# Performance work log

Measured on AMD Instinct MI355X. Metric: run time of the kernel, lower is better.

The kernel has to match this reference:

```python
import jax, jax.numpy as jnp
import numpy as np

THRESHOLD = 1.0  # LIF firing threshold (single-step LIF: spike = heaviside(v - thr))


def _lif_spike(v):
    # single-step LIF: membrane = input, spike where membrane exceeds threshold
    return (v > THRESHOLD).astype(v.dtype)


def setup_inputs() -> dict:
    key = jax.random.key(0)
    ks = jax.random.split(key, 9)
    B, T, C = 2, 2048, 1024
    s = 1.0 / np.sqrt(C)
    return {
        "x": jax.random.normal(ks[0], (B, T, C), dtype=jnp.float32),
        "Wq": jax.random.normal(ks[1], (C, C), dtype=jnp.float32) * s,
        "bq": jnp.zeros((C,), dtype=jnp.float32),
        "Wk": jax.random.normal(ks[2], (C, C), dtype=jnp.float32) * s,
        "bk": jnp.zeros((C,), dtype=jnp.float32),
        "Wv": jax.random.normal(ks[3], (C, C), dtype=jnp.float32) * s,
        "bv": jnp.zeros((C,), dtype=jnp.float32),
        "Wo": jax.random.normal(ks[4], (C, C), dtype=jnp.float32) * s,
        "bo": jnp.zeros((C,), dtype=jnp.float32),
    }


def reference(x, Wq, bq, Wk, bk, Wv, bv, Wo, bo):
    B, T, C = x.shape
    H = 16
    D = C // H
    q = x @ Wq.T + bq
    k = x @ Wk.T + bk
    v = x @ Wv.T + bv
    # LIF spiking on q and k (binary spikes)
    qs = _lif_spike(q).reshape(B, T, H, D).transpose(0, 2, 1, 3)  # [B,H,T,D]
    ks = _lif_spike(k).reshape(B, T, H, D).transpose(0, 2, 1, 3)  # [B,H,T,D]
    vh = v.reshape(B, T, H, D).transpose(0, 2, 1, 3)              # [B,H,T,D]
    scores = jnp.einsum('bhqd,bhkd->bhqk', qs, ks) / jnp.sqrt(jnp.asarray(D, x.dtype))
    attn = jax.nn.softmax(scores, axis=-1)
    out = jnp.einsum('bhqk,bhkd->bhqd', attn, vh)                 # [B,H,T,D]
    out = out.transpose(0, 2, 1, 3).reshape(B, T, C)
    return out @ Wo.T + bo
```

## Files before the change

### kernel.cpp

```cpp
#include <hip/hip_runtime.h>
#include <cstdint>

typedef unsigned long long u64;
typedef unsigned int u32;
typedef unsigned short u16;
typedef __attribute__((ext_vector_type(8))) u16 u16x8;
typedef __attribute__((ext_vector_type(4))) u16 u16x4;
typedef __attribute__((ext_vector_type(2))) u64 u64x2;
typedef __attribute__((ext_vector_type(8))) _Float16 f16x8;
typedef __attribute__((ext_vector_type(4))) float f32x4;

#define T_LEN 2048
#define C_DIM 1024
#define H_NUM 16
#define M_ROWS 4096
#define MB (1024ull * 1024ull)
#define TAU 3e-3f
#define FCAP 65536u
#define BLK_FCAP 512u

__device__ __forceinline__ u16 f2bf(float f) {
  unsigned u = __builtin_bit_cast(unsigned, f);
  return (u16)((u + 0x7FFFu + ((u >> 16) & 1u)) >> 16);
}
__device__ __forceinline__ u16 f2h(float f) {
  _Float16 h = (_Float16)f;
  return __builtin_bit_cast(u16, h);
}

__device__ __forceinline__ void async16(u16* lds, const u16* g) {
  __builtin_amdgcn_global_load_lds(
      (const __attribute__((address_space(1))) void*)g,
      (__attribute__((address_space(3))) void*)lds, 16, 0, 0);
}

__global__ __launch_bounds__(256) void split_all(
    const float* __restrict__ x,  const float* __restrict__ Wq,
    const float* __restrict__ Wk, const float* __restrict__ Wv,
    const float* __restrict__ Wo,
    u16* xh, u16* wq16, u16* wk16, u16* wv16, u16* woh, u32* flagcnt)
{
  const int i = blockIdx.x * 256 + threadIdx.x;
  if (i == 0) *flagcnt = 0;
  const float* src; u16* dst; int off; int isbf = 0;
  if      (i < 1048576) { src = x;  dst = xh;   off = i; }
  else if (i < 1310720) { src = Wq; dst = wq16; off = i - 1048576; }
  else if (i < 1572864) { src = Wk; dst = wk16; off = i - 1310720; }
  else if (i < 1835008) { src = Wv; dst = wv16; off = i - 1572864; }
  else                  { src = Wo; dst = woh;  off = i - 1835008; isbf = 1; }
  const float4 v = ((const float4*)src)[off];
  u16x4 h;
  if (isbf) {
    h[0] = f2bf(v.x); h[1] = f2bf(v.y); h[2] = f2bf(v.z); h[3] = f2bf(v.w);
  } else {
    h[0] = f2h(v.x);  h[1] = f2h(v.y);  h[2] = f2h(v.z);  h[3] = f2h(v.w);
  }
  ((u16x4*)dst)[off] = h;
}

__global__ __launch_bounds__(256) void mfma_qkv(
    const u16* __restrict__ A16,
    const u16* __restrict__ Bq16, const u16* __restrict__ Bk16,
    const u16* __restrict__ Bv16,
    const float* __restrict__ bq, const float* __restrict__ bk,
    const float* __restrict__ bv,
    u32* __restrict__ pbits, u32* __restrict__ flagcnt,
    u32* __restrict__ flaglist, u16* __restrict__ vT)
{
  __shared__ u16 Ahs[2][128][32];
  __shared__ u16 Bhs[2][128][32];
  __shared__ u32 fls[2 + BLK_FCAP];

  const int tid  = threadIdx.x;
  const int lane = tid & 63;
  const int w    = tid >> 6;
  const int wr   = w & 1;
  const int wc   = w >> 1;
  const int bm   = blockIdx.x * 128;
  const int bng  = blockIdx.y * 128;
  const int sel  = bng >> 10;
  const int bnl  = bng & 1023;

  const u16* Bh = (sel == 0) ? Bq16 : (sel == 1) ? Bk16 : Bv16;
  const float* bias = (sel == 0) ? bq : (sel == 1) ? bk : bv;

  if (tid == 0) fls[0] = 0;

  f32x4 acc[4][4];
  #pragma unroll
  for (int mf = 0; mf < 4; ++mf)
    #pragma unroll
    for (int nf = 0; nf < 4; ++nf) acc[mf][nf] = (f32x4){0.f, 0.f, 0.f, 0.f};

  const int sr = lane >> 2;
  const int sc = lane & 3;

#define STG(DST, SRC, TB, R0, KT)                                          \
  async16(&DST[(R0)][0],                                                   \
          &SRC[(size_t)((TB) + (R0) + sr) * 1024 + (KT) +                  \
               ((sc ^ ((((R0) + sr) >> 1) & 3)) << 3)]);

#define STAGE(B_, KT)                          \
  {                                            \
    STG(Ahs[B_], A16, bm, w * 32, KT);         \
    STG(Ahs[B_], A16, bm, w * 32 + 16, KT);    \
    STG(Bhs[B_], Bh, bnl, w * 32, KT);         \
    STG(Bhs[B_], Bh, bnl, w * 32 + 16, KT);    \
  }

  STAGE(0, 0);
  __syncthreads();

  const int fr = lane & 15;
  const int fg = lane >> 4;
  int cur = 0;

  for (int kt = 0; kt < 1024; kt += 32) {
    if (kt + 32 < 1024) STAGE(cur ^ 1, kt + 32);

    f16x8 a_h[4], b_h[4];
    #pragma unroll
    for (int mf = 0; mf < 4; ++mf) {
      const int row = wr * 64 + mf * 16 + fr;
      const int cs = (fg ^ ((row >> 1) & 3)) << 3;
      a_h[mf] = __builtin_bit_cast(f16x8, *(const u16x8*)&Ahs[cur][row][cs]);
    }
    #pragma unroll
    for (int nf = 0; nf < 4; ++nf) {
      const int col = wc * 64 + nf * 16 + fr;
      const int cs = (fg ^ ((col >> 1) & 3)) << 3;
      b_h[nf] = __builtin_bit_cast(f16x8, *(const u16x8*)&Bhs[cur][col][cs]);
    }
    #pragma unroll
    for (int mf = 0; mf < 4; ++mf)
      #pragma unroll
      for (int nf = 0; nf < 4; ++nf)
        acc[mf][nf] = __builtin_amdgcn_mfma_f32_16x16x32_f16(a_h[mf], b_h[nf], acc[mf][nf], 0, 0, 0);
    __syncthreads();
    cur ^= 1;
  }
#undef STAGE
#undef STG

  if (sel < 2) {
    float bb[4];
    #pragma unroll
    for (int nf = 0; nf < 4; ++nf) bb[nf] = bias[bnl + wc * 64 + nf * 16 + fr];
    #pragma unroll
    for (int mf = 0; mf < 4; ++mf) {
      const int row0 = bm + wr * 64 + mf * 16;
      #pragma unroll
      for (int j = 0; j < 4; ++j) {
        const int m = row0 + fg * 4 + j;
        float v[4];
        u64 bl[4];
        #pragma unroll
        for (int nf = 0; nf < 4; ++nf) {
          v[nf] = acc[mf][nf][j] + bb[nf];
          bl[nf] = __ballot(v[nf] > 1.0f);
        }
        if (fr == 0) {
          #pragma unroll
          for (int nfp = 0; nfp < 2; ++nfp) {
            const u32 mask = (u32)((bl[2 * nfp] >> (fg * 16)) & 0xFFFFu)
                           | ((u32)((bl[2 * nfp + 1] >> (fg * 16)) & 0xFFFFu) << 16);
            const int cb = bnl + wc * 64 + nfp * 32;
            pbits[(((size_t)sel * 4096 + m) * 16 + (cb >> 6)) * 2 + ((cb >> 5) & 1)] = mask;
          }
        }
        #pragma unroll
        for (int nf = 0; nf < 4; ++nf) {
          if (__builtin_fabsf(v[nf] - 1.0f) < TAU) {
            const u32 s = atomicAdd(&fls[0], 1u);
            const u32 cc = (u32)(bnl + wc * 64 + nf * 16 + fr);
            if (s < BLK_FCAP) fls[2 + s] = ((u32)sel << 22) | ((u32)m << 10) | cc;
          }
        }
      }
    }
    __syncthreads();
    const u32 cnt = fls[0] < BLK_FCAP ? fls[0] : BLK_FCAP;
    if (tid == 0) fls[1] = atomicAdd(flagcnt, cnt);
    __syncthreads();
    const u32 base = fls[1];
    for (u32 i = tid; i < cnt; i += 256) {
      const u32 pos = base + i;
      if (pos < FCAP) flaglist[pos] = fls[2 + i];
    }
  } else {
    #pragma unroll
    for (int mf = 0; mf < 4; ++mf) {
      const int row0 = bm + wr * 64 + mf * 16 + fg * 4;
      #pragma unroll
      for (int nf = 0; nf < 4; ++nf) {
        const int col = bnl + wc * 64 + nf * 16 + fr;
        const float bbv = bias[col];
        const int bb_ = row0 >> 11, t0 = row0 & 2047;
        const int hh = col >> 6, dd = col & 63;
        u16x4 o;
        o[0] = f2bf(acc[mf][nf][0] + bbv);
        o[1] = f2bf(acc[mf][nf][1] + bbv);
        o[2] = f2bf(acc[mf][nf][2] + bbv);
        o[3] = f2bf(acc[mf][nf][3] + bbv);
        *(u16x4*)&vT[(((size_t)(bb_ * 16 + hh)) * 64 + dd) * 2048 + t0] = o;
      }
    }
  }
}

__global__ __launch_bounds__(256) void fix_bits(
    const float* __restrict__ x,
    const float* __restrict__ Wq, const float* __restrict__ Wk,
    const float* __restrict__ bq, const float* __restrict__ bk,
    u32* __restrict__ pbits,
    const u32* __restrict__ flagcnt, const u32* __restrict__ flaglist)
{
  u32 cnt = *flagcnt;
  if (cnt > FCAP) cnt = FCAP;
  const int lane = threadIdx.x & 63;
  const u32 wid  = (blockIdx.x * 256 + threadIdx.x) >> 6;
  const u32 nw   = gridDim.x * 4;
  for (u32 i = wid; i < cnt; i += nw) {
    const u32 e = flaglist[i];
    const int which = e >> 22;
    const int m = (e >> 10) & 4095;
    const int n = e & 1023;
    const float* W    = which ? Wk : Wq;
    const float* bias = which ? bk : bq;
    float s = 0.f;
    #pragma unroll
    for (int j = 0; j < 16; ++j)
      s += x[(size_t)m * 1024 + lane + j * 64] * W[(size_t)n * 1024 + lane + j * 64];
    #pragma unroll
    for (int off = 32; off > 0; off >>= 1) s += __shfl_xor(s, off);
    const float val = s + bias[n];
    if (lane == 0) {
      const size_t idx = (((size_t)which * 4096 + m) * 16 + (n >> 6)) * 2 + ((n >> 5) & 1);
      const u32 bit = 1u << (n & 31);
      const bool oldb = (pbits[idx] >> (n & 31)) & 1u;
      const bool newb = val > 1.0f;
      if (oldb != newb) atomicXor(&pbits[idx], bit);
    }
  }
}

__global__ __launch_bounds__(256) void attn_mfma(
    const u32* __restrict__ pbits, const u16* __restrict__ vT,
    u16* __restrict__ oh)
{
  __shared__ u16 vtb[64][136];
  __shared__ u64 kbt[128];

  const int tid = threadIdx.x, lane = tid & 63, w = tid >> 6;
  const int bid = ((blockIdx.x & 7) << 7) | (blockIdx.x >> 3);
  const int qt = bid & 31, bh = bid >> 5, b = bh >> 4, h = bh & 15;

  const int fr = lane & 15, fg = lane >> 4;

  const int qm = b * T_LEN + qt * 64 + w * 16 + fr;
  const size_t qbase = (((size_t)qm) * 16 + h) * 2;
  const u32 qlo = pbits[qbase];
  const u32 qhi = pbits[qbase + 1];

  f32x4 acc[4];
  #pragma unroll
  for (int nf = 0; nf < 4; ++nf) acc[nf] = (f32x4){0.f, 0.f, 0.f, 0.f};
  f32x4 acc_z = (f32x4){0.f, 0.f, 0.f, 0.f};

  u16x8 ones;
  #pragma unroll
  for (int j = 0; j < 8; ++j) ones[j] = 0x3F80;

  const u16* vbase = vT + (size_t)bh * 64 * T_LEN;
  const int sd = tid >> 2, sk = (tid & 3) << 3;

  u16x8 r0, r1, r2, r3;
  u64 kbr = 0;
#define VLOAD(KT)                                                       \
  {                                                                     \
    r0 = *(const u16x8*)&vbase[(size_t)sd * T_LEN + (KT) + sk];         \
    r1 = *(const u16x8*)&vbase[(size_t)sd * T_LEN + (KT) + sk + 32];    \
    r2 = *(const u16x8*)&vbase[(size_t)sd * T_LEN + (KT) + sk + 64];    \
    r3 = *(const u16x8*)&vbase[(size_t)sd * T_LEN + (KT) + sk + 96];    \
  }
#define KLOAD(KT)                                                       \
  if (tid < 128) {                                                      \
    const int km = b * T_LEN + (KT) + tid;                              \
    const size_t kb = (((size_t)(4096 + km)) * 16 + h) * 2;             \
    kbr = (u64)pbits[kb] | ((u64)pbits[kb + 1] << 32);                  \
  }

  VLOAD(0);
  KLOAD(0);

  for (int kt = 0; kt < T_LEN; kt += 128) {
    *(u16x8*)&vtb[sd][sk]      = r0;
    *(u16x8*)&vtb[sd][sk + 32] = r1;
    *(u16x8*)&vtb[sd][sk + 64] = r2;
    *(u16x8*)&vtb[sd][sk + 96] = r3;
    if (tid < 128) kbt[tid] = kbr;
    if (kt + 128 < T_LEN) { VLOAD(kt + 128); KLOAD(kt + 128); }
    __syncthreads();

    __builtin_amdgcn_s_setprio(1);
    #pragma unroll
    for (int ks = 0; ks < 4; ++ks) {
      u64 kreg[8];
      const int kb0 = ks * 32 + fg * 8;
      *(u64x2*)&kreg[0] = *(const u64x2*)&kbt[kb0];
      *(u64x2*)&kreg[2] = *(const u64x2*)&kbt[kb0 + 2];
      *(u64x2*)&kreg[4] = *(const u64x2*)&kbt[kb0 + 4];
      *(u64x2*)&kreg[6] = *(const u64x2*)&kbt[kb0 + 6];
      u16x8 af;
      u32* afw = (u32*)&af;
      #pragma unroll
      for (int p = 0; p < 4; ++p) {
        const int mm0 = __builtin_popcount(qlo & (u32)kreg[2 * p])
                      + __builtin_popcount(qhi & (u32)(kreg[2 * p] >> 32));
        const int mm1 = __builtin_popcount(qlo & (u32)kreg[2 * p + 1])
                      + __builtin_popcount(qhi & (u32)(kreg[2 * p + 1] >> 32));
        const u32 t0 = __builtin_bit_cast(u32, exp2f((float)mm0 * 0.1803368801f));
        const u32 t1 = __builtin_bit_cast(u32, exp2f((float)mm1 * 0.1803368801f));
        afw[p] = (t1 & 0xFFFF0000u) | (t0 >> 16);
      }
      #pragma unroll
      for (int nf = 0; nf < 4; ++nf) {
        const u16x8 bfv = *(const u16x8*)&vtb[nf * 16 + fr][ks * 32 + fg * 8];
        acc[nf] = __builtin_amdgcn_mfma_f32_16x16x32_bf16(af, bfv, acc[nf], 0, 0, 0);
      }
      acc_z = __builtin_amdgcn_mfma_f32_16x16x32_bf16(af, ones, acc_z, 0, 0, 0);
    }
    __builtin_amdgcn_s_setprio(0);
    __syncthreads();
  }
#undef VLOAD
#undef KLOAD

  float invZ[4];
  #pragma unroll
  for (int j = 0; j < 4; ++j) invZ[j] = 1.0f / acc_z[j];

  #pragma unroll
  for (int nf = 0; nf < 4; ++nf) {
    const int col = h * 64 + nf * 16 + fr;
    #pragma unroll
    for (int j = 0; j < 4; ++j) {
      const int qrow = w * 16 + fg * 4 + j;
      const float o = acc[nf][j] * invZ[j];
      const size_t gq = (size_t)b * T_LEN + qt * 64 + qrow;
      oh[gq * 1024 + col] = f2bf(o);
    }
  }
}

__global__ __launch_bounds__(256) void mfma_out(
    const u16* __restrict__ Ah, const u16* __restrict__ Bh,
    const float* __restrict__ bias, float* __restrict__ out)
{
  __shared__ u16 Ahs[2][128][32];
  __shared__ u16 Bhs[2][64][32];

  const int tid  = threadIdx.x;
  const int lane = tid & 63;
  const int w    = tid >> 6;
  const int wr   = w & 1;
  const int wc   = w >> 1;
  const int bm   = blockIdx.x * 128;
  const int bn   = blockIdx.y * 64;

  f32x4 acc[4][2];
  #pragma unroll
  for (int mf = 0; mf < 4; ++mf)
    #pragma unroll
    for (int nf = 0; nf < 2; ++nf) acc[mf][nf] = (f32x4){0.f, 0.f, 0.f, 0.f};

  const int sr = lane >> 2;
  const int sc = lane & 3;

#define STG(DST, SRC, TB, R0, KT)                                          \
  async16(&DST[(R0)][0],                                                   \
          &SRC[(size_t)((TB) + (R0) + sr) * 1024 + (KT) +                  \
               ((sc ^ ((((R0) + sr) >> 1) & 3)) << 3)]);

#define STAGE(B_, KT)                        \
  {                                          \
    STG(Ahs[B_], Ah, bm, w * 32, KT);        \
    STG(Ahs[B_], Ah, bm, w * 32 + 16, KT);   \
    STG(Bhs[B_], Bh, bn, w * 16, KT);        \
  }

  STAGE(0, 0);
  __syncthreads();

  const int fr = lane & 15;
  const int fg = lane >> 4;
  int cur = 0;

  for (int kt = 0; kt < 1024; kt += 32) {
    if (kt + 32 < 1024) STAGE(cur ^ 1, kt + 32);

    u16x8 a_h[4], b_h[2];
    #pragma unroll
    for (int mf = 0; mf < 4; ++mf) {
      const int row = wr * 64 + mf * 16 + fr;
      const int cs = (fg ^ ((row >> 1) & 3)) << 3;
      a_h[mf] = *(const u16x8*)&Ahs[cur][row][cs];
    }
    #pragma unroll
    for (int nf = 0; nf < 2; ++nf) {
      const int col = wc * 32 + nf * 16 + fr;
      const int cs = (fg ^ ((col >> 1) & 3)) << 3;
      b_h[nf] = *(const u16x8*)&Bhs[cur][col][cs];
    }
    #pragma unroll
    for (int mf = 0; mf < 4; ++mf)
      #pragma unroll
      for (int nf = 0; nf < 2; ++nf)
        acc[mf][nf] = __builtin_amdgcn_mfma_f32_16x16x32_bf16(a_h[mf], b_h[nf], acc[mf][nf], 0, 0, 0);
    __syncthreads();
    cur ^= 1;
  }
#undef STAGE
#undef STG

  #pragma unroll
  for (int mf = 0; mf < 4; ++mf) {
    const int row0 = bm + wr * 64 + mf * 16 + fg * 4;
    #pragma unroll
    for (int nf = 0; nf < 2; ++nf) {
      const int col = bn + wc * 32 + nf * 16 + fr;
      const float bb = bias[col];
      #pragma unroll
      for (int j = 0; j < 4; ++j)
        out[(size_t)(row0 + j) * 1024 + col] = acc[mf][nf][j] + bb;
    }
  }
}

extern "C" void kernel_launch(void* const* d_in, const int* in_sizes, int n_in,
                              void* d_out, int out_size, void* d_ws, size_t ws_size,
                              hipStream_t stream) {
  const float* x  = (const float*)d_in[0];
  const float* Wq = (const float*)d_in[1];
  const float* bq = (const float*)d_in[2];
  const float* Wk = (const float*)d_in[3];
  const float* bk = (const float*)d_in[4];
  const float* Wv = (const float*)d_in[5];
  const float* bv = (const float*)d_in[6];
  const float* Wo = (const float*)d_in[7];
  const float* bo = (const float*)d_in[8];
  float* out = (float*)d_out;

  char* ws = (char*)d_ws;
  u16* oh   = (u16*)ws;
  u16* xh   = (u16*)(ws + 16 * MB);
  u16* vT   = (u16*)(ws + 32 * MB);
  u16* Woh  = (u16*)(ws + 40 * MB);
  u32* pbits = (u32*)(ws + 44 * MB);
  u32* flagcnt  = (u32*)(ws + 45 * MB);
  u32* flaglist = (u32*)(ws + 45 * MB + 256);

  char* dob = (char*)d_out;
  u16* Wq16 = (u16*)dob;
  u16* Wk16 = (u16*)(dob + 2 * MB);
  u16* Wv16 = (u16*)(dob + 4 * MB);

  split_all<<<8192, 256, 0, stream>>>(x, Wq, Wk, Wv, Wo,
                                      xh, Wq16, Wk16, Wv16, Woh, flagcnt);

  dim3 g1(M_ROWS / 128, 3072 / 128);
  mfma_qkv<<<g1, 256, 0, stream>>>(xh, Wq16, Wk16, Wv16,
                                   bq, bk, bv, pbits, flagcnt, flaglist, vT);

  fix_bits<<<256, 256, 0, stream>>>(x, Wq, Wk, bq, bk, pbits, flagcnt, flaglist);

  attn_mfma<<<32 * 32, 256, 0, stream>>>(pbits, vT, oh);

  dim3 g2(M_ROWS / 128, 1024 / 64);
  mfma_out<<<g2, 256, 0, stream>>>(oh, Woh, bo, out);
}
```

Measured before the change: 173.4 us.

## Halve attention key tile, pad key bit buffer, use exp lookup table

Shrinks the per-iteration key/value tile in the spiking attention kernel from 128 to 64 keys, which reduces LDS usage and register staging. It pads the key bitmask buffer to spread bank accesses and replaces per-element exp2f with a 65-entry shared-memory table indexed by the popcount match. This trades fewer transcendental ops and lower LDS pressure for twice as many barriers, narrower LDS loads and data-dependent table gathers.

```diff
diff --git a/kernel.cpp b/kernel.cpp
--- a/kernel.cpp
+++ b/kernel.cpp
@@ -6,7 +6,6 @@
 typedef unsigned short u16;
 typedef __attribute__((ext_vector_type(8))) u16 u16x8;
 typedef __attribute__((ext_vector_type(4))) u16 u16x4;
-typedef __attribute__((ext_vector_type(2))) u64 u64x2;
 typedef __attribute__((ext_vector_type(8))) _Float16 f16x8;
 typedef __attribute__((ext_vector_type(4))) float f32x4;
 
@@ -248,14 +247,18 @@
     const u32* __restrict__ pbits, const u16* __restrict__ vT,
     u16* __restrict__ oh)
 {
-  __shared__ u16 vtb[64][136];
-  __shared__ u64 kbt[128];
+  __shared__ u16 vtb[64][72];
+  __shared__ u64 kbt[68];
+  __shared__ u32 wt_tab[65];
 
   const int tid = threadIdx.x, lane = tid & 63, w = tid >> 6;
   const int bid = ((blockIdx.x & 7) << 7) | (blockIdx.x >> 3);
   const int qt = bid & 31, bh = bid >> 5, b = bh >> 4, h = bh & 15;
 
   const int fr = lane & 15, fg = lane >> 4;
+
+  if (tid < 65)
+    wt_tab[tid] = __builtin_bit_cast(u32, exp2f((float)tid * 0.1803368801f));
 
   const int qm = b * T_LEN + qt * 64 + w * 16 + fr;
   const size_t qbase = (((size_t)qm) * 16 + h) * 2;
@@ -274,17 +277,15 @@
   const u16* vbase = vT + (size_t)bh * 64 * T_LEN;
   const int sd = tid >> 2, sk = (tid & 3) << 3;
 
-  u16x8 r0, r1, r2, r3;
+  u16x8 r0, r1;
   u64 kbr = 0;
 #define VLOAD(KT)                                                       \
   {                                                                     \
     r0 = *(const u16x8*)&vbase[(size_t)sd * T_LEN + (KT) + sk];         \
     r1 = *(const u16x8*)&vbase[(size_t)sd * T_LEN + (KT) + sk + 32];    \
-    r2 = *(const u16x8*)&vbase[(size_t)sd * T_LEN + (KT) + sk + 64];    \
-    r3 = *(const u16x8*)&vbase[(size_t)sd * T_LEN + (KT) + sk + 96];    \
   }
 #define KLOAD(KT)                                                       \
-  if (tid < 128) {                                                      \
+  if (tid < 64) {                                                       \
     const int km = b * T_LEN + (KT) + tid;                              \
     const size_t kb = (((size_t)(4096 + km)) * 16 + h) * 2;             \
     kbr = (u64)pbits[kb] | ((u64)pbits[kb + 1] << 32);                  \
@@ -293,34 +294,30 @@
   VLOAD(0);
   KLOAD(0);
 
-  for (int kt = 0; kt < T_LEN; kt += 128) {
+  for (int kt = 0; kt < T_LEN; kt += 64) {
     *(u16x8*)&vtb[sd][sk]      = r0;
     *(u16x8*)&vtb[sd][sk + 32] = r1;
-    *(u16x8*)&vtb[sd][sk + 64] = r2;
-    *(u16x8*)&vtb[sd][sk + 96] = r3;
-    if (tid < 128) kbt[tid] = kbr;
-    if (kt + 128 < T_LEN) { VLOAD(kt + 128); KLOAD(kt + 128); }
+    if (tid < 64) kbt[tid + (tid >> 4)] = kbr;
+    if (kt + 64 < T_LEN) { VLOAD(kt + 64); KLOAD(kt + 64); }
     __syncthreads();
 
     __builtin_amdgcn_s_setprio(1);
     #pragma unroll
-    for (int ks = 0; ks < 4; ++ks) {
-      u64 kreg[8];
-      const int kb0 = ks * 32 + fg * 8;
-      *(u64x2*)&kreg[0] = *(const u64x2*)&kbt[kb0];
-      *(u64x2*)&kreg[2] = *(const u64x2*)&kbt[kb0 + 2];
-      *(u64x2*)&kreg[4] = *(const u64x2*)&kbt[kb0 + 4];
-      *(u64x2*)&kreg[6] = *(const u64x2*)&kbt[kb0 + 6];
+    for (int ks = 0; ks < 2; ++ks) {
       u16x8 af;
       u32* afw = (u32*)&af;
       #pragma unroll
       for (int p = 0; p < 4; ++p) {
-        const int mm0 = __builtin_popcount(qlo & (u32)kreg[2 * p])
-                      + __builtin_popcount(qhi & (u32)(kreg[2 * p] >> 32));
-        const int mm1 = __builtin_popcount(qlo & (u32)kreg[2 * p + 1])
-                      + __builtin_popcount(qhi & (u32)(kreg[2 * p + 1] >> 32));
-        const u32 t0 = __builtin_bit_cast(u32, exp2f((float)mm0 * 0.1803368801f));
-        const u32 t1 = __builtin_bit_cast(u32, exp2f((float)mm1 * 0.1803368801f));
+        const int kk = ks * 32 + fg * 8 + p * 2;
+        const int pidx = kk + (kk >> 4);
+        const u64 kb0 = kbt[pidx];
+        const u64 kb1 = kbt[pidx + 1];
+        const int mm0 = __builtin_popcount(qlo & (u32)kb0)
+                      + __builtin_popcount(qhi & (u32)(kb0 >> 32));
+        const int mm1 = __builtin_popcount(qlo & (u32)kb1)
+                      + __builtin_popcount(qhi & (u32)(kb1 >> 32));
+        const u32 t0 = wt_tab[mm0];
+        const u32 t1 = wt_tab[mm1];
         afw[p] = (t1 & 0xFFFF0000u) | (t0 >> 16);
       }
       #pragma unroll
```

New measurement: 165.5 us. -4.5%, faster.
